# Kernel tuning notes

Measured on AMD Instinct MI355X. Metric: run time of the kernel, lower is better.

Reference implementation:

```python
import jax, jax.numpy as jnp
import numpy as np

EPS = 1e-5

def layer_norm(x, g, b):
    mu = jnp.mean(x, axis=-1, keepdims=True)
    var = jnp.mean(jnp.square(x - mu), axis=-1, keepdims=True)
    return (x - mu) * jax.lax.rsqrt(var + EPS) * g + b

def setup_inputs() -> dict:
    key = jax.random.key(0)
    ks = jax.random.split(key, 16)
    B, S, D, H, T = 8, 1024, 512, 8, 6
    Dff = 4 * D
    s = 0.02
    return {
        "x": jax.random.normal(ks[0], (B, S, D), jnp.float32),
        "signal_type_ids": jax.random.randint(ks[1], (B, S), 0, T, jnp.int32),
        "emb": jax.random.normal(ks[2], (T, D), jnp.float32) * s,
        "in_proj_w": jax.random.normal(ks[3], (3 * D, D), jnp.float32) * s,
        "in_proj_b": jnp.zeros((3 * D,), jnp.float32),
        "out_proj_w": jax.random.normal(ks[4], (D, D), jnp.float32) * s,
        "out_proj_b": jnp.zeros((D,), jnp.float32),
        "ln1_g": jnp.ones((D,), jnp.float32),
        "ln1_b": jnp.zeros((D,), jnp.float32),
        "ln2_g": jnp.ones((D,), jnp.float32),
        "ln2_b": jnp.zeros((D,), jnp.float32),
        "w1": jax.random.normal(ks[5], (Dff, D), jnp.float32) * s,
        "b1": jnp.zeros((Dff,), jnp.float32),
        "w2": jax.random.normal(ks[6], (D, Dff), jnp.float32) * s,
        "b2": jnp.zeros((D,), jnp.float32),
    }

def reference(x, signal_type_ids, emb, in_proj_w, in_proj_b, out_proj_w, out_proj_b,
              ln1_g, ln1_b, ln2_g, ln2_b, w1, b1, w2, b2):
    B, S, D = x.shape
    H = 8
    hd = D // H
    # embedding add
    x = x + emb[signal_type_ids]
    # pre-norm MHA (need_weights=True path, average_attn_weights=True)
    xn = layer_norm(x, ln1_g, ln1_b)
    qkv = xn @ in_proj_w.T + in_proj_b            # [B,S,3D]
    q, k, v = jnp.split(qkv, 3, axis=-1)
    q = q.reshape(B, S, H, hd)
    k = k.reshape(B, S, H, hd)
    v = v.reshape(B, S, H, hd)
    scores = jnp.einsum("bqhd,bkhd->bhqk", q, k) / jnp.sqrt(jnp.asarray(hd, x.dtype))
    attn = jax.nn.softmax(scores, axis=-1)        # [B,H,S,S]
    attn_weights = jnp.mean(attn, axis=1)         # averaged over heads [B,S,S]
    ctx = jnp.einsum("bhqk,bkhd->bqhd", attn, v).reshape(B, S, D)
    attn_out = ctx @ out_proj_w.T + out_proj_b
    x = x + attn_out
    # FFN with exact GELU (torch nn.GELU default)
    h = layer_norm(x, ln2_g, ln2_b)
    h = jax.nn.gelu(h @ w1.T + b1, approximate=False)
    x = x + h @ w2.T + b2
    return x, attn_weights
```

## Files before the change

### kernel.cpp

```cpp
#include <hip/hip_runtime.h>
#include <math.h>

constexpr int CB = 8;
constexpr int CS = 1024;
constexpr int CD = 512;
constexpr int CH = 8;
constexpr int CHD = 64;
constexpr int CDFF = 2048;
constexpr int NROW = CB * CS;

typedef unsigned short u16;
typedef unsigned int u32;
typedef __attribute__((ext_vector_type(8))) short short8;
typedef __attribute__((ext_vector_type(8))) unsigned short ushort8v;
typedef __attribute__((ext_vector_type(4))) float floatx4;

__device__ inline u16 f2bf(float f) {
    union { float f; unsigned u; } v; v.f = f;
    unsigned u = v.u + 0x7FFFu + ((v.u >> 16) & 1u);
    return (u16)(u >> 16);
}
__device__ inline float bf2f(u16 h) {
    union { unsigned u; float f; } v; v.u = ((unsigned)h) << 16;
    return v.f;
}

__device__ inline float gelu_fast(float v) {
    float u = v * (1.0f + 0.044715f * v * v);
    float e = __expf(-1.5957691216057308f * u);
    return v / (1.0f + e);
}

__device__ inline void gload16(const u16* g, u16* l) {
    __builtin_amdgcn_global_load_lds(
        (const __attribute__((address_space(1))) u32*)g,
        (__attribute__((address_space(3))) u32*)l, 16, 0, 0);
}

__global__ __launch_bounds__(256) void ln_kernel(
    const float* __restrict__ x, const int* __restrict__ ids,
    const float* __restrict__ emb,
    const float* __restrict__ g, const float* __restrict__ beta,
    float* __restrict__ xr_out, u16* __restrict__ xn_out)
{
    __shared__ float red1[4], red2[4];
    __shared__ float mu_s, ri_s;
    int row = blockIdx.x;
    int tid = threadIdx.x;
    int d0 = tid * 2;
    const float* xrow = x + (size_t)row * CD;
    float2 xv = *(const float2*)(xrow + d0);
    float v0 = xv.x, v1 = xv.y;
    if (emb) {
        int id = ids[row];
        float2 ev = *(const float2*)(emb + (size_t)id * CD + d0);
        v0 += ev.x; v1 += ev.y;
    }
    float s1 = v0 + v1;
    float s2 = v0 * v0 + v1 * v1;
    for (int off = 32; off > 0; off >>= 1) {
        s1 += __shfl_down(s1, off, 64);
        s2 += __shfl_down(s2, off, 64);
    }
    int wave = tid >> 6;
    if ((tid & 63) == 0) { red1[wave] = s1; red2[wave] = s2; }
    __syncthreads();
    if (tid == 0) {
        float t1 = red1[0] + red1[1] + red1[2] + red1[3];
        float t2 = red2[0] + red2[1] + red2[2] + red2[3];
        float mu = t1 / CD;
        float var = t2 / CD - mu * mu;
        mu_s = mu;
        ri_s = rsqrtf(var + 1e-5f);
    }
    __syncthreads();
    float mu = mu_s, ri = ri_s;
    if (xr_out) {
        float2 o; o.x = v0; o.y = v1;
        *(float2*)(xr_out + (size_t)row * CD + d0) = o;
    }
    float2 gv = *(const float2*)(g + d0);
    float2 bv = *(const float2*)(beta + d0);
    float n0 = (v0 - mu) * ri * gv.x + bv.x;
    float n1 = (v1 - mu) * ri * gv.y + bv.y;
    u32 pk = (u32)f2bf(n0) | ((u32)f2bf(n1) << 16);
    *(u32*)(xn_out + (size_t)row * CD + d0) = pk;
}

__global__ __launch_bounds__(256) void conv4_kernel(
    const float* __restrict__ s0, const float* __restrict__ s1,
    const float* __restrict__ s2, const float* __restrict__ s3,
    u16* __restrict__ dst)
{
    size_t i = ((size_t)blockIdx.x * 256 + threadIdx.x) * 8;
    const float* src;
    size_t off;
    if (i < 786432)        { src = s0; off = i; }
    else if (i < 1048576)  { src = s1; off = i - 786432; }
    else if (i < 2097152)  { src = s2; off = i - 1048576; }
    else                   { src = s3; off = i - 2097152; }
    float4 a = *(const float4*)(src + off);
    float4 b = *(const float4*)(src + off + 4);
    ushort8v o;
    o[0] = f2bf(a.x); o[1] = f2bf(a.y); o[2] = f2bf(a.z); o[3] = f2bf(a.w);
    o[4] = f2bf(b.x); o[5] = f2bf(b.y); o[6] = f2bf(b.z); o[7] = f2bf(b.w);
    *(ushort8v*)(dst + i) = o;
}

template <int ACT, int RES, int OUTBF>
__global__ __launch_bounds__(256) void gemm_mfma(
    const u16* __restrict__ A, const u16* __restrict__ W,
    const float* __restrict__ bias, const float* __restrict__ res,
    void* __restrict__ Cout, int M, int N, int K)
{
    __shared__ u16 As[2][128 * 32];
    __shared__ u16 Bs[2][128 * 32];
    int t = threadIdx.x;
    int lane = t & 63;
    int w = t >> 6;
    int m0 = blockIdx.x * 128;
    int n0 = blockIdx.y * 128;
    int col = lane & 15;
    int quad = lane >> 4;
    int wm = w & 1, wn = w >> 1;
    int lo = w * 512;

    const u16* ag = A + (size_t)(m0 + (t >> 2)) * K + (t & 3) * 8;
    const u16* ag2 = ag + (size_t)64 * K;
    const u16* bg = W + (size_t)(n0 + (t >> 2)) * K + (t & 3) * 8;
    const u16* bg2 = bg + (size_t)64 * K;

    gload16(ag, As[0] + lo);
    gload16(ag2, As[0] + 2048 + lo);
    gload16(bg, Bs[0] + lo);
    gload16(bg2, Bs[0] + 2048 + lo);
    __syncthreads();

    floatx4 acc[4][4];
#pragma unroll
    for (int i = 0; i < 4; i++)
#pragma unroll
        for (int j = 0; j < 4; j++) acc[i][j] = (floatx4){0.f, 0.f, 0.f, 0.f};

    int nk = K >> 5;
    for (int kt = 0; kt < nk; kt++) {
        int cur = kt & 1;
        if (kt + 1 < nk) {
            int ko = (kt + 1) * 32;
            gload16(ag + ko, As[cur ^ 1] + lo);
            gload16(ag2 + ko, As[cur ^ 1] + 2048 + lo);
            gload16(bg + ko, Bs[cur ^ 1] + lo);
            gload16(bg2 + ko, Bs[cur ^ 1] + 2048 + lo);
        }
        short8 af[4], bf[4];
#pragma unroll
        for (int mi = 0; mi < 4; mi++)
            af[mi] = *(const short8*)&As[cur][(wm * 64 + mi * 16 + col) * 32 + quad * 8];
#pragma unroll
        for (int ni = 0; ni < 4; ni++)
            bf[ni] = *(const short8*)&Bs[cur][(wn * 64 + ni * 16 + col) * 32 + quad * 8];
#pragma unroll
        for (int mi = 0; mi < 4; mi++)
#pragma unroll
            for (int ni = 0; ni < 4; ni++)
                acc[mi][ni] = __builtin_amdgcn_mfma_f32_16x16x32_bf16(
                    af[mi], bf[ni], acc[mi][ni], 0, 0, 0);
        __syncthreads();
    }

#pragma unroll
    for (int mi = 0; mi < 4; mi++)
#pragma unroll
        for (int ni = 0; ni < 4; ni++) {
            int c = n0 + wn * 64 + ni * 16 + col;
            float bv = bias[c];
#pragma unroll
            for (int r = 0; r < 4; r++) {
                int m = m0 + wm * 64 + mi * 16 + quad * 4 + r;
                float v = acc[mi][ni][r] + bv;
                if (ACT == 1) v = gelu_fast(v);
                if (RES) v += res[(size_t)m * N + c];
                if (OUTBF) ((u16*)Cout)[(size_t)m * N + c] = f2bf(v);
                else       ((float*)Cout)[(size_t)m * N + c] = v;
            }
        }
}

template <int ACT, int RES, int OUTBF>
__global__ __launch_bounds__(256) void gemm_mfma64(
    const u16* __restrict__ A, const u16* __restrict__ W,
    const float* __restrict__ bias, const float* __restrict__ res,
    void* __restrict__ Cout, int M, int N, int K)
{
    __shared__ u16 As[2][64 * 32];
    __shared__ u16 Bs[2][128 * 32];
    int t = threadIdx.x;
    int lane = t & 63;
    int w = t >> 6;
    int m0 = blockIdx.x * 64;
    int n0 = blockIdx.y * 128;
    int col = lane & 15;
    int quad = lane >> 4;
    int lo = w * 512;

    const u16* ag = A + (size_t)(m0 + (t >> 2)) * K + (t & 3) * 8;
    const u16* bg = W + (size_t)(n0 + (t >> 2)) * K + (t & 3) * 8;
    const u16* bg2 = bg + (size_t)64 * K;

    gload16(ag, As[0] + lo);
    gload16(bg, Bs[0] + lo);
    gload16(bg2, Bs[0] + 2048 + lo);
    __syncthreads();

    floatx4 acc[4][2];
#pragma unroll
    for (int i = 0; i < 4; i++)
#pragma unroll
        for (int j = 0; j < 2; j++) acc[i][j] = (floatx4){0.f, 0.f, 0.f, 0.f};

    int nk = K >> 5;
    for (int kt = 0; kt < nk; kt++) {
        int cur = kt & 1;
        if (kt + 1 < nk) {
            int ko = (kt + 1) * 32;
            gload16(ag + ko, As[cur ^ 1] + lo);
            gload16(bg + ko, Bs[cur ^ 1] + lo);
            gload16(bg2 + ko, Bs[cur ^ 1] + 2048 + lo);
        }
        short8 af[4], bf[2];
#pragma unroll
        for (int mi = 0; mi < 4; mi++)
            af[mi] = *(const short8*)&As[cur][(mi * 16 + col) * 32 + quad * 8];
#pragma unroll
        for (int ni = 0; ni < 2; ni++)
            bf[ni] = *(const short8*)&Bs[cur][(w * 32 + ni * 16 + col) * 32 + quad * 8];
#pragma unroll
        for (int mi = 0; mi < 4; mi++)
#pragma unroll
            for (int ni = 0; ni < 2; ni++)
                acc[mi][ni] = __builtin_amdgcn_mfma_f32_16x16x32_bf16(
                    af[mi], bf[ni], acc[mi][ni], 0, 0, 0);
        __syncthreads();
    }

#pragma unroll
    for (int mi = 0; mi < 4; mi++)
#pragma unroll
        for (int ni = 0; ni < 2; ni++) {
            int c = n0 + w * 32 + ni * 16 + col;
            float bv = bias[c];
#pragma unroll
            for (int r = 0; r < 4; r++) {
                int m = m0 + mi * 16 + quad * 4 + r;
                float v = acc[mi][ni][r] + bv;
                if (ACT == 1) v = gelu_fast(v);
                if (RES) v += res[(size_t)m * N + c];
                if (OUTBF) ((u16*)Cout)[(size_t)m * N + c] = f2bf(v);
                else       ((float*)Cout)[(size_t)m * N + c] = v;
            }
        }
}

__global__ __launch_bounds__(256) void vt_kernel(
    const u16* __restrict__ qkvb, u16* __restrict__ vt)
{
    __shared__ u16 tile[64][72];
    int b = blockIdx.x >> 4;
    int s0 = (blockIdx.x & 15) * 64;
    int h = blockIdx.y;
    int t = threadIdx.x;
    int r = t >> 2;
    int c0 = (t & 3) * 16;
    const u16* src = qkvb + (size_t)(b * CS + s0 + r) * 1536 + 2 * CD + h * CHD + c0;
    *(ushort8v*)&tile[r][c0] = *(const ushort8v*)src;
    *(ushort8v*)&tile[r][c0 + 8] = *(const ushort8v*)(src + 8);
    __syncthreads();
    u16* dst = vt + (((size_t)b * CH + h) * CHD + r) * CS + s0 + c0;
    ushort8v lo, hi;
#pragma unroll
    for (int j = 0; j < 8; j++) { lo[j] = tile[c0 + j][r]; hi[j] = tile[c0 + 8 + j][r]; }
    *(ushort8v*)dst = lo;
    *(ushort8v*)(dst + 8) = hi;
}

__global__ __launch_bounds__(256, 2) void attn_fused_kernel(
    const u16* __restrict__ qkvb, const u16* __restrict__ vt,
    u16* __restrict__ Se, float* __restrict__ Lout,
    u16* __restrict__ ctx, int b0)
{
    __shared__ u16 Qs[2][64 * 32];
    __shared__ u16 Ks[2][2][64 * 32];
    __shared__ u16 Vs[2][2][64 * 32];
    __shared__ u16 S[64][72];
    __shared__ float rs[4][4][16];

    int t = threadIdx.x;
    int lane = t & 63;
    int w = t >> 6;
    int col = lane & 15;
    int quad = lane >> 4;
    int bid = blockIdx.x;
    int xcd = bid & 7;
    int j = bid >> 3;
    int bhl = xcd * 4 + (j >> 4);
    int qt = j & 15;
    int lb = bhl >> 3, h = bhl & 7;
    int b = b0 + lb;
    int q0 = qt * 64;
    int bh = b * CH + h;
    size_t splane = (size_t)(lb * CH + h) * CS * CS;

    int srow = t >> 2;
    int scol = (t & 3) * 8;

    const u16* ksrc0 = qkvb + (size_t)(b * CS + srow) * 1536 + CD + h * CHD + scol;
    const u16* vsrc0 = vt + ((size_t)bh * CHD + srow) * CS + scol;

    {
        const u16* qsrc = qkvb + (size_t)(b * CS + q0 + srow) * 1536 + h * CHD + scol;
        gload16(qsrc, Qs[0] + w * 512);
        gload16(qsrc + 32, Qs[1] + w * 512);
        gload16(ksrc0, Ks[0][0] + w * 512);
        gload16(ksrc0 + 32, Ks[0][1] + w * 512);
        gload16(vsrc0, Vs[0][0] + w * 512);
        gload16(vsrc0 + 32, Vs[0][1] + w * 512);
    }
    __syncthreads();

    short8 qf[2][4];
#pragma unroll
    for (int dsl = 0; dsl < 2; dsl++)
#pragma unroll
        for (int nq = 0; nq < 4; nq++)
            qf[dsl][nq] = *(const short8*)&Qs[dsl][(nq * 16 + col) * 32 + quad * 8];

    floatx4 acc[4];
#pragma unroll
    for (int i = 0; i < 4; i++) acc[i] = (floatx4){0.f, 0.f, 0.f, 0.f};
    float esum[4] = {0.f, 0.f, 0.f, 0.f};

    for (int kc = 0; kc < 16; kc++) {
        int cur = kc & 1;
        short8 kf0 = *(const short8*)&Ks[cur][0][(w * 16 + col) * 32 + quad * 8];
        short8 kf1 = *(const short8*)&Ks[cur][1][(w * 16 + col) * 32 + quad * 8];
#pragma unroll
        for (int nq = 0; nq < 4; nq++) {
            floatx4 c = {0.f, 0.f, 0.f, 0.f};
            c = __builtin_amdgcn_mfma_f32_16x16x32_bf16(kf0, qf[0][nq], c, 0, 0, 0);
            c = __builtin_amdgcn_mfma_f32_16x16x32_bf16(kf1, qf[1][nq], c, 0, 0, 0);
            float e0 = __expf(c[0] * 0.125f);
            float e1 = __expf(c[1] * 0.125f);
            float e2 = __expf(c[2] * 0.125f);
            float e3 = __expf(c[3] * 0.125f);
            esum[nq] += (e0 + e1) + (e2 + e3);
            union { float f; u32 u; } a0, a1, a2, a3;
            a0.f = e0; a1.f = e1; a2.f = e2; a3.f = e3;
            u32 p0 = (a0.u >> 16) | (a1.u & 0xFFFF0000u);
            u32 p1 = (a2.u >> 16) | (a3.u & 0xFFFF0000u);
            u32* sp = (u32*)&S[nq * 16 + col][w * 16 + quad * 4];
            sp[0] = p0; sp[1] = p1;
            u32* gp = (u32*)(Se + splane + (size_t)(q0 + nq * 16 + col) * CS
                             + kc * 64 + w * 16 + quad * 4);
            gp[0] = p0; gp[1] = p1;
        }
        __syncthreads();

        if (kc < 15) {
            int ko = (kc + 1) * 64;
            const u16* ks = ksrc0 + (size_t)ko * 1536;
            gload16(ks, Ks[cur ^ 1][0] + w * 512);
            gload16(ks + 32, Ks[cur ^ 1][1] + w * 512);
            gload16(vsrc0 + ko, Vs[cur ^ 1][0] + w * 512);
            gload16(vsrc0 + ko + 32, Vs[cur ^ 1][1] + w * 512);
        }

        short8 sf0 = *(const short8*)&S[w * 16 + col][quad * 8];
        short8 sf1 = *(const short8*)&S[w * 16 + col][32 + quad * 8];
#pragma unroll
        for (int nd = 0; nd < 4; nd++) {
            short8 vf0 = *(const short8*)&Vs[cur][0][(nd * 16 + col) * 32 + quad * 8];
            short8 vf1 = *(const short8*)&Vs[cur][1][(nd * 16 + col) * 32 + quad * 8];
            acc[nd] = __builtin_amdgcn_mfma_f32_16x16x32_bf16(sf0, vf0, acc[nd], 0, 0, 0);
            acc[nd] = __builtin_amdgcn_mfma_f32_16x16x32_bf16(sf1, vf1, acc[nd], 0, 0, 0);
        }
        __syncthreads();
    }

#pragma unroll
    for (int nq = 0; nq < 4; nq++) {
        float v = esum[nq];
        v += __shfl_xor(v, 16, 64);
        v += __shfl_xor(v, 32, 64);
        if (quad == 0) rs[w][nq][col] = v;
    }
    __syncthreads();
    if (t < 64) {
        int nq = t >> 4, c2 = t & 15;
        float L = rs[0][nq][c2] + rs[1][nq][c2] + rs[2][nq][c2] + rs[3][nq][c2];
        Lout[((size_t)bh << 10) + q0 + nq * 16 + c2] = L;
    }

    float li[4];
#pragma unroll
    for (int r = 0; r < 4; r++) {
        int cr = quad * 4 + r;
        li[r] = 1.0f / (rs[0][w][cr] + rs[1][w][cr] + rs[2][w][cr] + rs[3][w][cr]);
    }
    u16* cb = ctx + ((size_t)(b * CS) + q0 + w * 16 + quad * 4) * CD + h * CHD + col;
#pragma unroll
    for (int nd = 0; nd < 4; nd++)
#pragma unroll
        for (int r = 0; r < 4; r++)
            cb[(size_t)r * CD + nd * 16] = f2bf(acc[nd][r] * li[r]);
}

__global__ __launch_bounds__(256, 8) void attn_aw_kernel(
    const u16* __restrict__ Se, const float* __restrict__ Lin,
    float* __restrict__ aw_out, int b0)
{
    int bq = blockIdx.x;
    int bl = bq >> 9;
    int b = b0 + bl;
    int q = (bq & 511) * 2 + (threadIdx.x >> 7);
    int k0 = (threadIdx.x & 127) * 8;

    float acc[8];
#pragma unroll
    for (int i = 0; i < 8; i++) acc[i] = 0.f;

#pragma unroll
    for (int h = 0; h < CH; h++) {
        float linv = 0.125f / Lin[(((size_t)(b * CH + h)) << 10) + q];
        const u16* sp = Se + ((size_t)(bl * CH + h) * CS + q) * CS + k0;
        ushort8v e = *(const ushort8v*)sp;
#pragma unroll
        for (int i = 0; i < 8; i++) acc[i] += bf2f(e[i]) * linv;
    }
    float* ap = aw_out + ((size_t)(b * CS) + q) * CS + k0;
    *(float4*)ap = make_float4(acc[0], acc[1], acc[2], acc[3]);
    *(float4*)(ap + 4) = make_float4(acc[4], acc[5], acc[6], acc[7]);
}

extern "C" void kernel_launch(void* const* d_in, const int* in_sizes, int n_in,
                              void* d_out, int out_size, void* d_ws, size_t ws_size,
                              hipStream_t stream)
{
    const float* x    = (const float*)d_in[0];
    const int*   ids  = (const int*)d_in[1];
    const float* emb  = (const float*)d_in[2];
    const float* inw  = (const float*)d_in[3];
    const float* inb  = (const float*)d_in[4];
    const float* ow   = (const float*)d_in[5];
    const float* ob   = (const float*)d_in[6];
    const float* g1   = (const float*)d_in[7];
    const float* be1  = (const float*)d_in[8];
    const float* g2   = (const float*)d_in[9];
    const float* be2  = (const float*)d_in[10];
    const float* w1   = (const float*)d_in[11];
    const float* b1   = (const float*)d_in[12];
    const float* w2   = (const float*)d_in[13];
    const float* b2   = (const float*)d_in[14];

    float* out_x  = (float*)d_out;
    float* out_aw = out_x + (size_t)CB * CS * CD;

    char* p = (char*)d_ws;
    float* xr   = (float*)p; p += (size_t)NROW * CD * 4;
    float* x2   = (float*)p; p += (size_t)NROW * CD * 4;
    u16* xnb    = (u16*)p;   p += (size_t)NROW * CD * 2;
    u16* qkvb   = (u16*)p;   p += (size_t)NROW * 3 * CD * 2;
    u16* ctxb   = (u16*)p;   p += (size_t)NROW * CD * 2;
    u16* hidb   = (u16*)p;   p += (size_t)NROW * CDFF * 2;
    u16* inwb   = (u16*)p;   p += (size_t)3 * CD * CD * 2;
    u16* owb    = (u16*)p;   p += (size_t)CD * CD * 2;
    u16* w1b    = (u16*)p;   p += (size_t)CDFF * CD * 2;
    u16* w2b    = (u16*)p;   p += (size_t)CD * CDFF * 2;
    float* Lbuf = (float*)p; p += (size_t)CB * CH * CS * 4;
    u16* Se     = (u16*)p;   p += (size_t)(CB / 2) * CH * CS * CS * 2;

    u16* vtb = hidb;

    dim3 blk(256);
    conv4_kernel<<<(3 * CD * CD + CD * CD + 2 * CDFF * CD) / 2048, blk, 0, stream>>>(
        inw, ow, w1, w2, inwb);
    ln_kernel<<<NROW, blk, 0, stream>>>(x, ids, emb, g1, be1, xr, xnb);
    gemm_mfma<0, 0, 1><<<dim3(NROW / 128, (3 * CD) / 128), blk, 0, stream>>>(
        xnb, inwb, inb, nullptr, qkvb, NROW, 3 * CD, CD);
    vt_kernel<<<dim3(CB * (CS / 64), CH), blk, 0, stream>>>(qkvb, vtb);
    for (int half = 0; half < 2; half++) {
        int b0 = half * 4;
        attn_fused_kernel<<<512, blk, 0, stream>>>(qkvb, vtb, Se, Lbuf, ctxb, b0);
        attn_aw_kernel<<<2048, blk, 0, stream>>>(Se, Lbuf, out_aw, b0);
    }
    gemm_mfma64<0, 1, 0><<<dim3(NROW / 64, CD / 128), blk, 0, stream>>>(
        ctxb, owb, ob, xr, x2, NROW, CD, CD);
    ln_kernel<<<NROW, blk, 0, stream>>>(x2, nullptr, nullptr, g2, be2, nullptr, xnb);
    gemm_mfma<1, 0, 1><<<dim3(NROW / 128, CDFF / 128), blk, 0, stream>>>(
        xnb, w1b, b1, nullptr, hidb, NROW, CDFF, CD);
    gemm_mfma64<0, 1, 0><<<dim3(NROW / 64, CD / 128), blk, 0, stream>>>(
        hidb, w2b, b2, x2, out_x, NROW, CD, CDFF);
}
```

Measured before the change: 315.2 us.

## Prefetch two K-tiles ahead with counted vmcnt waits in GEMM kernels

Both bf16 MFMA GEMM kernels now issue the first two K-tiles up front and, inside the loop, wait with a partial s_waitcnt vmcnt so only the current tile's global-to-LDS loads must complete, rather than draining every outstanding load at __syncthreads. The next refill is issued after the compute barrier into the buffer just consumed. The aim is to keep one tile of loads in flight during MFMA work and hide global latency. The manual waitcnt counts assume exactly 4 or 3 loads per stage, so any change to the loads or to compiler-emitted memory ops could break correctness.

```diff
diff --git a/kernel.cpp b/kernel.cpp
--- a/kernel.cpp
+++ b/kernel.cpp
@@ -35,6 +35,12 @@
     __builtin_amdgcn_global_load_lds(
         (const __attribute__((address_space(1))) u32*)g,
         (__attribute__((address_space(3))) u32*)l, 16, 0, 0);
+}
+
+__device__ inline void barrier_raw() {
+    asm volatile("" ::: "memory");
+    __builtin_amdgcn_s_barrier();
+    asm volatile("" ::: "memory");
 }
 
 __global__ __launch_bounds__(256) void ln_kernel(
@@ -134,7 +140,10 @@
     gload16(ag2, As[0] + 2048 + lo);
     gload16(bg, Bs[0] + lo);
     gload16(bg2, Bs[0] + 2048 + lo);
-    __syncthreads();
+    gload16(ag + 32, As[1] + lo);
+    gload16(ag2 + 32, As[1] + 2048 + lo);
+    gload16(bg + 32, Bs[1] + lo);
+    gload16(bg2 + 32, Bs[1] + 2048 + lo);
 
     floatx4 acc[4][4];
 #pragma unroll
@@ -145,13 +154,9 @@
     int nk = K >> 5;
     for (int kt = 0; kt < nk; kt++) {
         int cur = kt & 1;
-        if (kt + 1 < nk) {
-            int ko = (kt + 1) * 32;
-            gload16(ag + ko, As[cur ^ 1] + lo);
-            gload16(ag2 + ko, As[cur ^ 1] + 2048 + lo);
-            gload16(bg + ko, Bs[cur ^ 1] + lo);
-            gload16(bg2 + ko, Bs[cur ^ 1] + 2048 + lo);
-        }
+        if (kt == nk - 1) asm volatile("s_waitcnt vmcnt(0)" ::: "memory");
+        else              asm volatile("s_waitcnt vmcnt(4)" ::: "memory");
+        barrier_raw();
         short8 af[4], bf[4];
 #pragma unroll
         for (int mi = 0; mi < 4; mi++)
@@ -165,7 +170,14 @@
             for (int ni = 0; ni < 4; ni++)
                 acc[mi][ni] = __builtin_amdgcn_mfma_f32_16x16x32_bf16(
                     af[mi], bf[ni], acc[mi][ni], 0, 0, 0);
-        __syncthreads();
+        barrier_raw();
+        if (kt + 2 < nk) {
+            int ko = (kt + 2) * 32;
+            gload16(ag + ko, As[cur] + lo);
+            gload16(ag2 + ko, As[cur] + 2048 + lo);
+            gload16(bg + ko, Bs[cur] + lo);
+            gload16(bg2 + ko, Bs[cur] + 2048 + lo);
+        }
     }
 
 #pragma unroll
@@ -210,7 +222,9 @@
     gload16(ag, As[0] + lo);
     gload16(bg, Bs[0] + lo);
     gload16(bg2, Bs[0] + 2048 + lo);
-    __syncthreads();
+    gload16(ag + 32, As[1] + lo);
+    gload16(bg + 32, Bs[1] + lo);
+    gload16(bg2 + 32, Bs[1] + 2048 + lo);
 
     floatx4 acc[4][2];
 #pragma unroll
@@ -221,12 +235,9 @@
     int nk = K >> 5;
     for (int kt = 0; kt < nk; kt++) {
         int cur = kt & 1;
-        if (kt + 1 < nk) {
-            int ko = (kt + 1) * 32;
-            gload16(ag + ko, As[cur ^ 1] + lo);
-            gload16(bg + ko, Bs[cur ^ 1] + lo);
-            gload16(bg2 + ko, Bs[cur ^ 1] + 2048 + lo);
-        }
+        if (kt == nk - 1) asm volatile("s_waitcnt vmcnt(0)" ::: "memory");
+        else              asm volatile("s_waitcnt vmcnt(3)" ::: "memory");
+        barrier_raw();
         short8 af[4], bf[2];
 #pragma unroll
         for (int mi = 0; mi < 4; mi++)
@@ -240,7 +251,13 @@
             for (int ni = 0; ni < 2; ni++)
                 acc[mi][ni] = __builtin_amdgcn_mfma_f32_16x16x32_bf16(
                     af[mi], bf[ni], acc[mi][ni], 0, 0, 0);
-        __syncthreads();
+        barrier_raw();
+        if (kt + 2 < nk) {
+            int ko = (kt + 2) * 32;
+            gload16(ag + ko, As[cur] + lo);
+            gload16(bg + ko, Bs[cur] + lo);
+            gload16(bg2 + ko, Bs[cur] + 2048 + lo);
+        }
     }
 
 #pragma unroll
```

Result: no change. 319.0 us (+1.2%).
